# Optimization experiments

Hardware: AMD Instinct MI355X
Metric: run time of the kernel (lower is better)

Reference implementation:

```python
import jax, jax.numpy as jnp
import numpy as np

B, N, M = 4, 8192, 8192


def setup_inputs() -> dict:
    key = jax.random.key(0)
    k1, k2 = jax.random.split(key)
    xyz1 = jax.random.normal(k1, (B, N, 3), dtype=jnp.float32)
    xyz2 = jax.random.normal(k2, (B, M, 3), dtype=jnp.float32)
    return {"xyz1": xyz1, "xyz2": xyz2}


def _chamfer(xyz1, xyz2):
    # Squared Euclidean pairwise distances via the expansion
    # ||a-b||^2 = ||a||^2 + ||b||^2 - 2 a.b  (avoids a [B,N,M,3] diff tensor).
    sq1 = jnp.sum(xyz1 * xyz1, axis=-1)              # [B,N]
    sq2 = jnp.sum(xyz2 * xyz2, axis=-1)              # [B,M]
    inner = jnp.einsum('bnd,bmd->bnm', xyz1, xyz2)   # [B,N,M]
    d = sq1[:, :, None] + sq2[:, None, :] - 2.0 * inner
    d = jnp.maximum(d, 0.0)
    dist1 = jnp.min(d, axis=2)  # [B,N] nearest xyz2 point for each xyz1 point
    dist2 = jnp.min(d, axis=1)  # [B,M] nearest xyz1 point for each xyz2 point
    return dist1, dist2


def reference(xyz1, xyz2):
    return _chamfer(xyz1, xyz2)
```

## Files before the change

### kernel.cpp

```cpp
#include <hip/hip_runtime.h>


typedef __bf16 bf16_t;
typedef __bf16 bf16x8 __attribute__((ext_vector_type(8)));
typedef float  f32x16 __attribute__((ext_vector_type(16)));

#define NPTS    8192
#define NB      4
#define NSETPTS (NB * NPTS)
#define TPB     256
#define WAVES   4
#define QC      (WAVES * 32)
#define QPANELS (NPTS / QC)
#define SEGR    2
#define RC      (NPTS / SEGR)
#define RT      (RC / 32)

__global__ void chamfer_init_out(unsigned int* __restrict__ out, int n) {
    int i = blockIdx.x * blockDim.x + threadIdx.x;
    if (i < n) out[i] = 0x7F800000u;
}

__device__ __forceinline__ void split2(float v, bf16_t& h, bf16_t& l) {
    h = (bf16_t)v;
    l = (bf16_t)(v - (float)h);
}

__global__ void chamfer_prep(const float* __restrict__ xyz1,
                             const float* __restrict__ xyz2,
                             bf16_t* __restrict__ a16,
                             bf16_t* __restrict__ b16) {
    int i = blockIdx.x * blockDim.x + threadIdx.x;
    const float* src = (i >= NSETPTS) ? xyz2 : xyz1;
    int p = i & (NSETPTS - 1);
    float x = src[3 * p], y = src[3 * p + 1], z = src[3 * p + 2];
    float sq = x * x + y * y + z * z;

    bf16_t m2xh, m2xl, m2yh, m2yl, m2zh, m2zl;
    split2(-2.f * x, m2xh, m2xl);
    split2(-2.f * y, m2yh, m2yl);
    split2(-2.f * z, m2zh, m2zl);
    bf16_t xh, xl, yh, yl, zh, zl;
    split2(x, xh, xl); split2(y, yh, yl); split2(z, zh, zl);
    bf16_t sqh, sql;
    split2(sq, sqh, sql);
    bf16_t one = (bf16_t)1.0f, zero = (bf16_t)0.0f;

    bf16_t A[16]  = { m2xh, m2yh, m2zh,  m2xl, m2yl, m2zl,
                      m2xh, m2yh, m2zh,  sqh, sql, one, one, zero, zero, zero };
    bf16_t Bv[16] = { xh, yh, zh,  xh, yh, zh,  xl, yl, zl,
                      one, one, sqh, sql, zero, zero, zero };

    const int perm[16] = {0,1,2,3, 8,9,10,11, 4,5,6,7, 12,13,14,15};
    bf16_t* ao = a16 + (size_t)i * 16;
    bf16_t* bo = b16 + (size_t)i * 16;
#pragma unroll
    for (int j = 0; j < 16; ++j) { ao[j] = A[perm[j]]; bo[j] = Bv[perm[j]]; }
}

__global__ __launch_bounds__(TPB, 4) void chamfer_main(
    const bf16_t* __restrict__ a16,
    const bf16_t* __restrict__ b16,
    unsigned int* __restrict__ out)
{
    __shared__ float red[WAVES][32][33];

    int bid = blockIdx.x;
    int s   = bid & (SEGR - 1);    bid >>= 1;
    int qp  = bid & (QPANELS - 1); bid >>= 6;
    int b   = bid & 3;             bid >>= 2;
    int dir = bid;

    int wave = threadIdx.x >> 6;
    int lane = threadIdx.x & 63;
    int col  = lane & 31;
    int h    = lane >> 5;

    const bf16_t* ap = a16 + ((size_t)dir * NB + b) * NPTS * 16;
    const bf16_t* bp = b16 + ((size_t)(1 - dir) * NB + b) * NPTS * 16;

    int qbase = qp * QC + wave * 32;
    bf16x8 af = *((const bf16x8*)(ap + (size_t)(qbase + col) * 16) + h);

    const bf16x8* bptr = (const bf16x8*)(bp + (size_t)(s * RC) * 16) + h;
    const bf16x8* bl = bptr + col * 2;

    f32x16 rm, zacc;
#pragma unroll
    for (int g = 0; g < 16; ++g) { rm[g] = INFINITY; zacc[g] = 0.f; }

    bf16x8 c0 = bl[0 * 64];
    bf16x8 c1 = bl[1 * 64];
    bf16x8 d0 = bl[2 * 64];
    bf16x8 d1 = bl[3 * 64];
    for (int t = 0; t < RT; t += 2) {
        int n0 = (t + 4 < RT) ? (t + 4) : 0;
        int n1 = (t + 5 < RT) ? (t + 5) : 0;
        bf16x8 p0 = bl[(size_t)n0 * 64];
        bf16x8 p1 = bl[(size_t)n1 * 64];

        f32x16 a0 = __builtin_amdgcn_mfma_f32_32x32x16_bf16(af, c0, zacc, 0, 0, 0);
        f32x16 a1 = __builtin_amdgcn_mfma_f32_32x32x16_bf16(af, c1, zacc, 0, 0, 0);
#pragma unroll
        for (int g = 0; g < 16; ++g)
            rm[g] = fminf(fminf(a0[g], a1[g]), rm[g]);

        c0 = d0; c1 = d1;
        d0 = p0; d1 = p1;
    }

#pragma unroll
    for (int g = 0; g < 16; ++g) {
        int row = (g & 3) + 8 * (g >> 2) + 4 * h;
        red[wave][row][col] = rm[g];
    }
    __syncthreads();

    if (threadIdx.x < QC) {
        int w = threadIdx.x >> 5, r = threadIdx.x & 31;
        const float* rp = &red[w][r][0];
        float v0 = rp[0], v1 = rp[1], v2 = rp[2], v3 = rp[3];
#pragma unroll
        for (int c = 4; c < 32; c += 4) {
            v0 = fminf(v0, rp[c + 0]);
            v1 = fminf(v1, rp[c + 1]);
            v2 = fminf(v2, rp[c + 2]);
            v3 = fminf(v3, rp[c + 3]);
        }
        float v = fmaxf(fminf(fminf(v0, v1), fminf(v2, v3)), 0.f);
        unsigned idx = (unsigned)(dir * NSETPTS + b * NPTS + qp * QC + threadIdx.x);
        atomicMin(&out[idx], __float_as_uint(v));
    }
}

extern "C" void kernel_launch(void* const* d_in, const int* in_sizes, int n_in,
                              void* d_out, int out_size, void* d_ws, size_t ws_size,
                              hipStream_t stream) {
    const float* xyz1 = (const float*)d_in[0];
    const float* xyz2 = (const float*)d_in[1];
    unsigned int* out = (unsigned int*)d_out;

    bf16_t* a16 = (bf16_t*)d_ws;
    bf16_t* b16 = a16 + (size_t)2 * NSETPTS * 16;

    hipLaunchKernelGGL(chamfer_init_out,
                       dim3((out_size + TPB - 1) / TPB), dim3(TPB), 0, stream,
                       out, out_size);

    hipLaunchKernelGGL(chamfer_prep,
                       dim3(2 * NSETPTS / TPB), dim3(TPB), 0, stream,
                       xyz1, xyz2, a16, b16);

    hipLaunchKernelGGL(chamfer_main,
                       dim3(2 * NB * QPANELS * SEGR), dim3(TPB), 0, stream,
                       a16, b16, out);
}
```

Baseline: 84.96 us.

## Stage reference tile in LDS and compute four query tiles per wave

Each wave now processes four 32-query tiles instead of one, reusing each loaded reference fragment across four MFMAs. The reference segment for a block (1024 points) is copied once into LDS with global_load_lds, using an XOR-swizzled layout written by the prep kernel to avoid bank conflicts. SEGR grows from 2 to 8 so the grid stays large, and the reduction runs four passes. This targets the global-load bandwidth per MFMA, at the cost of more registers (four accumulators, launch_bounds occupancy hint dropped), 32KB LDS per block, more atomics per output, and extra syncs in the epilogue.

New measurement: 84.53 us. Within noise of the previous version (-0.5%).

```diff
diff --git a/kernel.cpp b/kernel.cpp
--- a/kernel.cpp
+++ b/kernel.cpp
@@ -10,15 +10,23 @@
 #define NSETPTS (NB * NPTS)
 #define TPB     256
 #define WAVES   4
-#define QC      (WAVES * 32)
+#define QPW     4
+#define QC      (WAVES * QPW * 32)
 #define QPANELS (NPTS / QC)
-#define SEGR    2
+#define SEGR    8
 #define RC      (NPTS / SEGR)
 #define RT      (RC / 32)
+#define NSLOT   (RC * 2)
 
 __global__ void chamfer_init_out(unsigned int* __restrict__ out, int n) {
     int i = blockIdx.x * blockDim.x + threadIdx.x;
     if (i < n) out[i] = 0x7F800000u;
+}
+
+__device__ __forceinline__ void gload16(const bf16_t* g, bf16_t* l) {
+    __builtin_amdgcn_global_load_lds(
+        (const __attribute__((address_space(1))) void*)g,
+        (__attribute__((address_space(3))) void*)l, 16, 0, 0);
 }
 
 __device__ __forceinline__ void split2(float v, bf16_t& h, bf16_t& l) {
@@ -32,8 +40,8 @@
                              bf16_t* __restrict__ b16) {
     int i = blockIdx.x * blockDim.x + threadIdx.x;
     const float* src = (i >= NSETPTS) ? xyz2 : xyz1;
-    int p = i & (NSETPTS - 1);
-    float x = src[3 * p], y = src[3 * p + 1], z = src[3 * p + 2];
+    int p32 = i & (NSETPTS - 1);
+    float x = src[3 * p32], y = src[3 * p32 + 1], z = src[3 * p32 + 2];
     float sq = x * x + y * y + z * z;
 
     bf16_t m2xh, m2xl, m2yh, m2yl, m2zh, m2zl;
@@ -52,22 +60,35 @@
                       one, one, sqh, sql, zero, zero, zero };
 
     const int perm[16] = {0,1,2,3, 8,9,10,11, 4,5,6,7, 12,13,14,15};
+
     bf16_t* ao = a16 + (size_t)i * 16;
-    bf16_t* bo = b16 + (size_t)i * 16;
-#pragma unroll
-    for (int j = 0; j < 16; ++j) { ao[j] = A[perm[j]]; bo[j] = Bv[perm[j]]; }
-}
-
-__global__ __launch_bounds__(TPB, 4) void chamfer_main(
+#pragma unroll
+    for (int j = 0; j < 16; ++j) ao[j] = A[perm[j]];
+
+    int p = i & 31;
+    size_t tb = (size_t)(i & ~31) * 16;
+    int s0 = (2 * p)     ^ (p & 7);
+    int s1 = (2 * p + 1) ^ (p & 7);
+    bf16_t* bo0 = b16 + tb + (size_t)s0 * 8;
+    bf16_t* bo1 = b16 + tb + (size_t)s1 * 8;
+#pragma unroll
+    for (int j = 0; j < 8; ++j) bo0[j] = Bv[perm[j]];
+#pragma unroll
+    for (int j = 0; j < 8; ++j) bo1[j] = Bv[perm[j + 8]];
+}
+
+__global__ __launch_bounds__(TPB) void chamfer_main(
     const bf16_t* __restrict__ a16,
     const bf16_t* __restrict__ b16,
     unsigned int* __restrict__ out)
 {
-    __shared__ float red[WAVES][32][33];
+    __shared__ __align__(16) unsigned char smem[NSLOT * 16];
+    bf16_t* sbuf = (bf16_t*)smem;
+    float (*red)[32][33] = (float (*)[32][33])smem;
 
     int bid = blockIdx.x;
-    int s   = bid & (SEGR - 1);    bid >>= 1;
-    int qp  = bid & (QPANELS - 1); bid >>= 6;
+    int s   = bid & (SEGR - 1);    bid >>= 3;
+    int qp  = bid & (QPANELS - 1); bid >>= 4;
     int b   = bid & 3;             bid >>= 2;
     int dir = bid;
 
@@ -78,59 +99,98 @@
 
     const bf16_t* ap = a16 + ((size_t)dir * NB + b) * NPTS * 16;
     const bf16_t* bp = b16 + ((size_t)(1 - dir) * NB + b) * NPTS * 16;
-
-    int qbase = qp * QC + wave * 32;
-    bf16x8 af = *((const bf16x8*)(ap + (size_t)(qbase + col) * 16) + h);
-
-    const bf16x8* bptr = (const bf16x8*)(bp + (size_t)(s * RC) * 16) + h;
-    const bf16x8* bl = bptr + col * 2;
-
-    f32x16 rm, zacc;
-#pragma unroll
-    for (int g = 0; g < 16; ++g) { rm[g] = INFINITY; zacc[g] = 0.f; }
-
-    bf16x8 c0 = bl[0 * 64];
-    bf16x8 c1 = bl[1 * 64];
-    bf16x8 d0 = bl[2 * 64];
-    bf16x8 d1 = bl[3 * 64];
+    const bf16_t* gB = bp + (size_t)(s * RC) * 16;
+
+#pragma unroll
+    for (int c = 0; c < 8; ++c) {
+        int slot = c * 256 + threadIdx.x;
+        gload16(gB + (size_t)slot * 8, sbuf + (size_t)slot * 8);
+    }
+
+    int qbase = qp * QC + wave * (QPW * 32);
+    bf16x8 af0 = *((const bf16x8*)(ap + (size_t)(qbase +  0 + col) * 16) + h);
+    bf16x8 af1 = *((const bf16x8*)(ap + (size_t)(qbase + 32 + col) * 16) + h);
+    bf16x8 af2 = *((const bf16x8*)(ap + (size_t)(qbase + 64 + col) * 16) + h);
+    bf16x8 af3 = *((const bf16x8*)(ap + (size_t)(qbase + 96 + col) * 16) + h);
+
+    f32x16 rm0, rm1, rm2, rm3, zacc;
+#pragma unroll
+    for (int g = 0; g < 16; ++g) {
+        rm0[g] = INFINITY; rm1[g] = INFINITY;
+        rm2[g] = INFINITY; rm3[g] = INFINITY; zacc[g] = 0.f;
+    }
+
+    __syncthreads();
+
+    int swz = ((2 * col + h) ^ (col & 7)) * 8;
+    const bf16_t* sl = sbuf + swz;
+
+    bf16x8 c0 = *(const bf16x8*)(sl + 0 * 512);
+    bf16x8 c1 = *(const bf16x8*)(sl + 1 * 512);
     for (int t = 0; t < RT; t += 2) {
-        int n0 = (t + 4 < RT) ? (t + 4) : 0;
-        int n1 = (t + 5 < RT) ? (t + 5) : 0;
-        bf16x8 p0 = bl[(size_t)n0 * 64];
-        bf16x8 p1 = bl[(size_t)n1 * 64];
-
-        f32x16 a0 = __builtin_amdgcn_mfma_f32_32x32x16_bf16(af, c0, zacc, 0, 0, 0);
-        f32x16 a1 = __builtin_amdgcn_mfma_f32_32x32x16_bf16(af, c1, zacc, 0, 0, 0);
-#pragma unroll
-        for (int g = 0; g < 16; ++g)
-            rm[g] = fminf(fminf(a0[g], a1[g]), rm[g]);
-
-        c0 = d0; c1 = d1;
-        d0 = p0; d1 = p1;
-    }
-
-#pragma unroll
-    for (int g = 0; g < 16; ++g) {
-        int row = (g & 3) + 8 * (g >> 2) + 4 * h;
-        red[wave][row][col] = rm[g];
-    }
+        bf16x8 p0, p1;
+        if (t + 2 < RT) {
+            p0 = *(const bf16x8*)(sl + (t + 2) * 512);
+            p1 = *(const bf16x8*)(sl + (t + 3) * 512);
+        } else { p0 = c0; p1 = c1; }
+
+        f32x16 x0 = __builtin_amdgcn_mfma_f32_32x32x16_bf16(af0, c0, zacc, 0, 0, 0);
+        f32x16 x1 = __builtin_amdgcn_mfma_f32_32x32x16_bf16(af0, c1, zacc, 0, 0, 0);
+#pragma unroll
+        for (int g = 0; g < 16; ++g) rm0[g] = fminf(fminf(x0[g], x1[g]), rm0[g]);
+
+        f32x16 x2 = __builtin_amdgcn_mfma_f32_32x32x16_bf16(af1, c0, zacc, 0, 0, 0);
+        f32x16 x3 = __builtin_amdgcn_mfma_f32_32x32x16_bf16(af1, c1, zacc, 0, 0, 0);
+#pragma unroll
+        for (int g = 0; g < 16; ++g) rm1[g] = fminf(fminf(x2[g], x3[g]), rm1[g]);
+
+        f32x16 x4 = __builtin_amdgcn_mfma_f32_32x32x16_bf16(af2, c0, zacc, 0, 0, 0);
+        f32x16 x5 = __builtin_amdgcn_mfma_f32_32x32x16_bf16(af2, c1, zacc, 0, 0, 0);
+#pragma unroll
+        for (int g = 0; g < 16; ++g) rm2[g] = fminf(fminf(x4[g], x5[g]), rm2[g]);
+
+        f32x16 x6 = __builtin_amdgcn_mfma_f32_32x32x16_bf16(af3, c0, zacc, 0, 0, 0);
+        f32x16 x7 = __builtin_amdgcn_mfma_f32_32x32x16_bf16(af3, c1, zacc, 0, 0, 0);
+#pragma unroll
+        for (int g = 0; g < 16; ++g) rm3[g] = fminf(fminf(x6[g], x7[g]), rm3[g]);
+
+        c0 = p0; c1 = p1;
+    }
+
     __syncthreads();
-
-    if (threadIdx.x < QC) {
-        int w = threadIdx.x >> 5, r = threadIdx.x & 31;
-        const float* rp = &red[w][r][0];
-        float v0 = rp[0], v1 = rp[1], v2 = rp[2], v3 = rp[3];
-#pragma unroll
-        for (int c = 4; c < 32; c += 4) {
-            v0 = fminf(v0, rp[c + 0]);
-            v1 = fminf(v1, rp[c + 1]);
-            v2 = fminf(v2, rp[c + 2]);
-            v3 = fminf(v3, rp[c + 3]);
-        }
-        float v = fmaxf(fminf(fminf(v0, v1), fminf(v2, v3)), 0.f);
-        unsigned idx = (unsigned)(dir * NSETPTS + b * NPTS + qp * QC + threadIdx.x);
-        atomicMin(&out[idx], __float_as_uint(v));
-    }
+    int outbase = dir * NSETPTS + b * NPTS + qp * QC;
+
+#define RED_PASS(QT, RM)                                                      \
+    {                                                                         \
+        _Pragma("unroll")                                                     \
+        for (int g = 0; g < 16; ++g) {                                        \
+            int row = (g & 3) + 8 * (g >> 2) + 4 * h;                         \
+            red[wave][row][col] = RM[g];                                      \
+        }                                                                     \
+        __syncthreads();                                                      \
+        if (threadIdx.x < 128) {                                              \
+            int w = threadIdx.x >> 5, r = threadIdx.x & 31;                   \
+            const float* rp = &red[w][r][0];                                  \
+            float v0 = rp[0], v1 = rp[1], v2 = rp[2], v3 = rp[3];             \
+            _Pragma("unroll")                                                 \
+            for (int cc = 4; cc < 32; cc += 4) {                              \
+                v0 = fminf(v0, rp[cc + 0]);                                   \
+                v1 = fminf(v1, rp[cc + 1]);                                   \
+                v2 = fminf(v2, rp[cc + 2]);                                   \
+                v3 = fminf(v3, rp[cc + 3]);                                   \
+            }                                                                 \
+            float v = fmaxf(fminf(fminf(v0, v1), fminf(v2, v3)), 0.f);        \
+            atomicMin(&out[outbase + w * (QPW * 32) + (QT) * 32 + r],         \
+                      __float_as_uint(v));                                    \
+        }                                                                     \
+        __syncthreads();                                                      \
+    }
+
+    RED_PASS(0, rm0)
+    RED_PASS(1, rm1)
+    RED_PASS(2, rm2)
+    RED_PASS(3, rm3)
+#undef RED_PASS
 }
 
 extern "C" void kernel_launch(void* const* d_in, const int* in_sizes, int n_in,
```
